# Optimization experiments

Measured on AMD Instinct MI355X. Metric: run time of the kernel, lower is better.

The kernel has to match this reference:

```python
import jax, jax.numpy as jnp
import numpy as np

PARAM = 10.0
EPS = 1e-10

def delu(x):
    # delu_feature_map: param*relu(x) + (exp(param*min(x,0)) - 1) + 1
    return PARAM * jax.nn.relu(x) + jnp.expm1(PARAM * jnp.minimum(x, 0.0)) + 1.0

def conv1x1(x, w, b):
    # x: (B,C,H,W), w: (O,C), b: (O,)
    return jnp.einsum('oc,bchw->bohw', w, x) + b[None, :, None, None]

def conv3x3(x, w, b):
    # x: (B,C,H,W), w: (O,C,3,3)
    y = jax.lax.conv_general_dilated(x, w, window_strides=(1, 1), padding='SAME',
                                     dimension_numbers=('NCHW', 'OIHW', 'NCHW'))
    return y + b[None, :, None, None]

def setup_inputs() -> dict:
    key = jax.random.key(0)
    B, C, H, W = 4, 256, 128, 128
    ks = jax.random.split(key, 20)
    s = 0.05
    d = {
        'x1': jax.random.normal(ks[0], (B, C, H, W), jnp.float32),
        'x2': jax.random.normal(ks[1], (B, C, H, W), jnp.float32),
        'wq1': jax.random.normal(ks[2], (C, C), jnp.float32) * s,
        'bq1': jax.random.normal(ks[3], (C,), jnp.float32) * s,
        'wk1': jax.random.normal(ks[4], (C, C), jnp.float32) * s,
        'bk1': jax.random.normal(ks[5], (C,), jnp.float32) * s,
        'wv1': jax.random.normal(ks[6], (C, C), jnp.float32) * s,
        'bv1': jax.random.normal(ks[7], (C,), jnp.float32) * s,
        'wq2': jax.random.normal(ks[8], (C, C), jnp.float32) * s,
        'bq2': jax.random.normal(ks[9], (C,), jnp.float32) * s,
        'wk2': jax.random.normal(ks[10], (C, C), jnp.float32) * s,
        'bk2': jax.random.normal(ks[11], (C,), jnp.float32) * s,
        'wv2': jax.random.normal(ks[12], (C, C), jnp.float32) * s,
        'bv2': jax.random.normal(ks[13], (C,), jnp.float32) * s,
        'wd1': jax.random.normal(ks[14], (C, C), jnp.float32) * s,
        'bd1': jax.random.normal(ks[15], (C,), jnp.float32) * s,
        'wd3': jax.random.normal(ks[16], (C, C, 3, 3), jnp.float32) * s,
        'bd3': jax.random.normal(ks[17], (C,), jnp.float32) * s,
        'gamma1': jax.random.normal(ks[18], (1,), jnp.float32) * 0.5,
        'gamma2': jax.random.normal(ks[19], (1,), jnp.float32) * 0.5,
    }
    return d

def reference(x1, x2, wq1, bq1, wk1, bk1, wv1, bv1, wq2, bq2, wk2, bk2,
              wv2, bv2, wd1, bd1, wd3, bd3, gamma1, gamma2):
    B, C, H, W = x1.shape
    N = H * W
    # QKV projections (1x1 convs), flattened to (B,C,N). delu is elementwise,
    # so applying it on (B,C,N) equals the permute/delu/permute in torch.
    q1 = delu(conv1x1(x1, wq1, bq1).reshape(B, C, N))
    k1 = delu(conv1x1(x1, wk1, bk1).reshape(B, C, N))
    v1 = conv1x1(x1, wv1, bv1).reshape(B, C, N)
    q2 = delu(conv1x1(x2, wq2, bq2).reshape(B, C, N))
    k2 = delu(conv1x1(x2, wk2, bk2).reshape(B, C, N))
    v2 = conv1x1(x2, wv2, bv2).reshape(B, C, N)

    # energy: (B,C,C) cross-kernel matrices
    energy1 = jnp.einsum('bmn,bcn->bmc', q1, k2)
    energy2 = jnp.einsum('bmn,bcn->bmc', q2, k1)

    KV1 = k1 * v1  # (B,C,N)
    KV2 = k2 * v2

    # norm: 1 / (sum_{m,c} energy[b,m,c] * k[b,c,n] + eps) -> (B,N)
    esum1 = energy1.sum(axis=1)  # (B,C)
    esum2 = energy2.sum(axis=1)
    norm1 = 1.0 / (jnp.einsum('bc,bcn->bn', esum1, k2) + EPS)
    norm2 = 1.0 / (jnp.einsum('bc,bcn->bn', esum2, k1) + EPS)

    # einsum('bmc,bcn,bn->bcn') factorizes: sum over m hits only energy
    att1 = (esum1[:, :, None] * KV1 * norm1[:, None, :]).reshape(B, C, H, W)
    att2 = (esum2[:, :, None] * KV2 * norm2[:, None, :]).reshape(B, C, H, W)

    out1 = att1 + conv1x1(x1, wd1, bd1) + conv3x3(x1, wd3, bd3)
    out2 = att2 + conv1x1(x2, wd1, bd1) + conv3x3(x2, wd3, bd3)
    out1 = x1 + gamma1[0] * out1
    out2 = x2 + gamma2[0] * out2
    return (out1, out2)
```

## Files before the change

### kernel.cpp

```cpp
#include <hip/hip_runtime.h>
#include <stdint.h>

#define Bn 4
#define Cn 256
#define Hn 128
#define Wn 128
#define Nn 16384
#define EPSn 1e-10f

typedef unsigned short u16;
typedef __attribute__((ext_vector_type(8))) short short8;
typedef __attribute__((ext_vector_type(4))) short short4v;
typedef __attribute__((ext_vector_type(4))) float f32x4;

#define GLOAD_LDS16(g, l)                                                        \
    __builtin_amdgcn_global_load_lds(                                            \
        (const __attribute__((address_space(1))) unsigned int*)(const void*)(g), \
        (__attribute__((address_space(3))) unsigned int*)(void*)(l), 16, 0, 0)

#define MFMA16(a, b, c) __builtin_amdgcn_mfma_f32_16x16x32_bf16(a, b, c, 0, 0, 0)

__device__ __forceinline__ float bf2f(u16 u) {
    union { float f; uint32_t i; } v; v.i = ((uint32_t)u) << 16; return v.f;
}
__device__ __forceinline__ u16 f2bf(float f) {
    union { float f; uint32_t i; } v; v.f = f;
    uint32_t r = v.i + 0x7FFFu + ((v.i >> 16) & 1u);
    return (u16)(r >> 16);
}
__device__ __forceinline__ float delu_f(float x) {
    return x >= 0.f ? fmaf(10.f, x, 1.f) : __expf(10.f * x);
}

__global__ void prep_kernel(const float* __restrict__ wq1, const float* __restrict__ wk1,
                            const float* __restrict__ wv1,
                            const float* __restrict__ wq2, const float* __restrict__ wk2,
                            const float* __restrict__ wv2,
                            const float* __restrict__ wd1, const float* __restrict__ wd3,
                            const float* __restrict__ bd1, const float* __restrict__ bd3,
                            const float* __restrict__ gamma1, const float* __restrict__ gamma2,
                            u16* __restrict__ wq1p, u16* __restrict__ wk1p, u16* __restrict__ wv1p,
                            u16* __restrict__ wq2p, u16* __restrict__ wk2p, u16* __restrict__ wv2p,
                            u16* __restrict__ wallp1, u16* __restrict__ wallp2,
                            float* __restrict__ bfused)
{
    int idx = blockIdx.x * 256 + threadIdx.x;
    int o = idx >> 8, c = idx & 255;
    if (idx < 256) bfused[idx] = bd1[idx] + bd3[idx];
    int s = o >> 6, mf = (o >> 4) & 3, lr = o & 15;
    int kc = c >> 5, lk = (c >> 3) & 3, j = c & 7;
    int poff = ((kc * 4 + s) * 4 + mf) * 512 + (lk * 16 + lr) * 8 + j;
    wq1p[poff] = f2bf(wq1[idx]);
    wk1p[poff] = f2bf(wk1[idx]);
    wv1p[poff] = f2bf(wv1[idx]);
    wq2p[poff] = f2bf(wq2[idx]);
    wk2p[poff] = f2bf(wk2[idx]);
    wv2p[poff] = f2bf(wv2[idx]);
    float wd1v = wd1[idx];
    float inv1 = 1.f / gamma1[0];
    float inv2 = 1.f / gamma2[0];
    float diag = (o == c) ? 1.f : 0.f;
    #pragma unroll
    for (int tap = 0; tap < 9; ++tap) {
        float w = wd3[idx * 9 + tap] + (tap == 4 ? wd1v : 0.f);
        wallp1[tap * 65536 + poff] = f2bf(w + (tap == 4 ? diag * inv1 : 0.f));
        wallp2[tap * 65536 + poff] = f2bf(w + (tap == 4 ? diag * inv2 : 0.f));
    }
}

__global__ void transpose_kernel(const float* __restrict__ x1, const float* __restrict__ x2,
                                 u16* __restrict__ xT1, u16* __restrict__ xT2)
{
    __shared__ __align__(16) u16 tl[64][72];
    int t = threadIdx.x;
    int z = blockIdx.z, img = z >> 2, b = z & 3;
    const float* x = img ? x2 : x1;
    u16* xT = img ? xT2 : xT1;
    int n0 = blockIdx.x * 64, c0 = blockIdx.y * 64;
    int cl = t >> 4, nl = (t & 15) * 4;
    #pragma unroll
    for (int pc = 0; pc < 4; ++pc) {
        int c = pc * 16 + cl;
        float4 v = *(const float4*)&x[((size_t)(b * Cn + c0 + c)) * Nn + n0 + nl];
        tl[nl + 0][c] = f2bf(v.x);
        tl[nl + 1][c] = f2bf(v.y);
        tl[nl + 2][c] = f2bf(v.z);
        tl[nl + 3][c] = f2bf(v.w);
    }
    __syncthreads();
    #pragma unroll
    for (int ps = 0; ps < 2; ++ps) {
        int id = ps * 256 + t;
        int nr = id >> 3, cc = (id & 7) * 8;
        short8 v = *(const short8*)&tl[nr][cc];
        *(short8*)&xT[((size_t)(b * Nn + n0 + nr)) * 256 + c0 + cc] = v;
    }
}

__global__ __launch_bounds__(256, 3) void qkv_kernel(
    const u16* __restrict__ xT1, const u16* __restrict__ xT2,
    const u16* __restrict__ wq1p, const u16* __restrict__ wk1p, const u16* __restrict__ wv1p,
    const u16* __restrict__ wq2p, const u16* __restrict__ wk2p, const u16* __restrict__ wv2p,
    const float* __restrict__ bq1, const float* __restrict__ bk1, const float* __restrict__ bv1,
    const float* __restrict__ bq2, const float* __restrict__ bk2, const float* __restrict__ bv2,
    u16* __restrict__ k1, u16* __restrict__ k2,
    u16* __restrict__ kv1, u16* __restrict__ kv2,
    float* __restrict__ qsum1, float* __restrict__ qsum2)
{
    __shared__ __align__(16) u16 Bt[2 * 2048];
    __shared__ __align__(16) u16 obuf[128 * 64];
    int t = threadIdx.x;
    int nb = blockIdx.x, mb = blockIdx.y;
    int z = blockIdx.z, img = z >> 2, b = z & 3;
    const u16* xT  = img ? xT2  : xT1;
    const u16* wqp = img ? wq2p : wq1p;
    const u16* wkp = img ? wk2p : wk1p;
    const u16* wvp = img ? wv2p : wv1p;
    const float* bq = img ? bq2 : bq1;
    const float* bk = img ? bk2 : bk1;
    const float* bv = img ? bv2 : bv1;
    u16* kout  = img ? k2  : k1;
    u16* kvout = img ? kv2 : kv1;
    float* qsum = img ? qsum2 : qsum1;

    int n0 = nb * 64;
    int lane = t & 63, wid = t >> 6;
    int wm = wid >> 1, wn = wid & 1;
    int lr = lane & 15, lk = lane >> 4;
    int s = mb * 2 + wm;

    f32x4 zf = {0.f, 0.f, 0.f, 0.f};
    f32x4 accq[4][2], acck[4][2], accv[4][2];
    #pragma unroll
    for (int i = 0; i < 4; ++i)
        #pragma unroll
        for (int j = 0; j < 2; ++j) { accq[i][j] = zf; acck[i][j] = zf; accv[i][j] = zf; }

    int colp = lane >> 2, chp = (lane & 3) * 8;
    auto STAGE = [&](int bufi, int kc) {
        const u16* g = xT + ((size_t)(b * Nn + n0 + wid * 16 + colp)) * 256 + kc * 32 + chp;
        GLOAD_LDS16(g, &Bt[bufi * 2048 + (wid * 16) * 32]);
    };

    STAGE(0, 0);
    __syncthreads();

    for (int kc = 0; kc < 8; ++kc) {
        int cur = kc & 1;
        if (kc < 7) STAGE(cur ^ 1, kc + 1);
        int abase = ((kc * 4 + s) * 4) * 512 + lane * 8;
        short8 bf[2];
        #pragma unroll
        for (int nf = 0; nf < 2; ++nf)
            bf[nf] = *(const short8*)&Bt[cur * 2048 + (wn * 32 + nf * 16 + lr) * 32 + lk * 8];
        #pragma unroll
        for (int mf = 0; mf < 4; ++mf) {
            short8 aq = *(const short8*)&wqp[abase + mf * 512];
            short8 ak = *(const short8*)&wkp[abase + mf * 512];
            short8 av = *(const short8*)&wvp[abase + mf * 512];
            __builtin_amdgcn_s_setprio(1);
            #pragma unroll
            for (int nf = 0; nf < 2; ++nf) {
                accq[mf][nf] = MFMA16(aq, bf[nf], accq[mf][nf]);
                acck[mf][nf] = MFMA16(ak, bf[nf], acck[mf][nf]);
                accv[mf][nf] = MFMA16(av, bf[nf], accv[mf][nf]);
            }
            __builtin_amdgcn_s_setprio(0);
        }
        __syncthreads();
    }

    float qs[2] = {0.f, 0.f};
    #pragma unroll
    for (int mf = 0; mf < 4; ++mf) {
        #pragma unroll
        for (int r = 0; r < 4; ++r) {
            int o = mb * 128 + wm * 64 + mf * 16 + lk * 4 + r;
            float bqv = bq[o];
            #pragma unroll
            for (int nf = 0; nf < 2; ++nf)
                qs[nf] += delu_f(accq[mf][nf][r] + bqv);
        }
    }
    #pragma unroll
    for (int nf = 0; nf < 2; ++nf) {
        float sgl = qs[nf];
        sgl += __shfl_xor(sgl, 16);
        sgl += __shfl_xor(sgl, 32);
        if (lk == 0)
            atomicAdd(&qsum[b * Nn + n0 + wn * 32 + nf * 16 + lr], sgl);
    }

    #pragma unroll
    for (int mf = 0; mf < 4; ++mf) {
        #pragma unroll
        for (int r = 0; r < 4; ++r) {
            int ol = wm * 64 + mf * 16 + lk * 4 + r;
            float bkv = bk[mb * 128 + ol];
            #pragma unroll
            for (int nf = 0; nf < 2; ++nf)
                obuf[ol * 64 + wn * 32 + nf * 16 + lr] = f2bf(delu_f(acck[mf][nf][r] + bkv));
        }
    }
    __syncthreads();
    #pragma unroll
    for (int i = 0; i < 4; ++i) {
        int sid = t * 4 + i;
        int o = sid >> 3, seg = sid & 7;
        short8 v = *(const short8*)&obuf[o * 64 + seg * 8];
        *(short8*)&kout[((size_t)(b * Cn + mb * 128 + o)) * Nn + n0 + seg * 8] = v;
    }
    __syncthreads();

    #pragma unroll
    for (int mf = 0; mf < 4; ++mf) {
        #pragma unroll
        for (int r = 0; r < 4; ++r) {
            int ol = wm * 64 + mf * 16 + lk * 4 + r;
            float bkv = bk[mb * 128 + ol];
            float bvv = bv[mb * 128 + ol];
            #pragma unroll
            for (int nf = 0; nf < 2; ++nf) {
                float kk = delu_f(acck[mf][nf][r] + bkv);
                float vv = accv[mf][nf][r] + bvv;
                obuf[ol * 64 + wn * 32 + nf * 16 + lr] = f2bf(kk * vv);
            }
        }
    }
    __syncthreads();
    #pragma unroll
    for (int i = 0; i < 4; ++i) {
        int sid = t * 4 + i;
        int o = sid >> 3, seg = sid & 7;
        short8 v = *(const short8*)&obuf[o * 64 + seg * 8];
        *(short8*)&kvout[((size_t)(b * Cn + mb * 128 + o)) * Nn + n0 + seg * 8] = v;
    }
}

__global__ void esum_kernel(const u16* __restrict__ k1, const u16* __restrict__ k2,
                            const float* __restrict__ qsum1, const float* __restrict__ qsum2,
                            float* __restrict__ esum1, float* __restrict__ esum2)
{
    int c = blockIdx.x, b = blockIdx.y, pair = blockIdx.z, t = threadIdx.x;
    const u16* k = pair ? k1 : k2;
    const float* qsum = pair ? qsum2 : qsum1;
    float* esum = pair ? esum2 : esum1;
    const u16* kr = k + ((size_t)(b * Cn + c)) * Nn;
    const float* qr = qsum + b * Nn;
    float s = 0.f;
    for (int i = t * 8; i < Nn; i += 2048) {
        short8 kv = *(const short8*)&kr[i];
        #pragma unroll
        for (int j = 0; j < 8; ++j) s = fmaf(bf2f((u16)kv[j]), qr[i + j], s);
    }
    #pragma unroll
    for (int m = 32; m; m >>= 1) s += __shfl_xor(s, m);
    __shared__ float red[4];
    if ((t & 63) == 0) red[t >> 6] = s;
    __syncthreads();
    if (t == 0) esum[b * Cn + c] = red[0] + red[1] + red[2] + red[3];
}

__global__ void norm_kernel(const u16* __restrict__ k1, const u16* __restrict__ k2,
                            const float* __restrict__ esum1, const float* __restrict__ esum2,
                            float* __restrict__ norm1, float* __restrict__ norm2)
{
    __shared__ float es[256];
    int t = threadIdx.x, b = blockIdx.y, pair = blockIdx.z;
    const u16* k = pair ? k1 : k2;
    const float* esum = pair ? esum2 : esum1;
    float* nrm = pair ? norm2 : norm1;
    es[t] = esum[b * Cn + t];
    __syncthreads();
    int n = blockIdx.x * 256 + t;
    const u16* kb = k + (size_t)b * Cn * Nn + n;
    float a = 0.f;
    #pragma unroll 8
    for (int c = 0; c < 256; ++c)
        a = fmaf(es[c], bf2f(kb[(size_t)c * Nn]), a);
    nrm[b * Nn + n] = 1.f / (a + EPSn);
}

#define BSZ6 (6 * 130 * 32)

__global__ __launch_bounds__(512, 2) void conv_att_kernel(
    const u16* __restrict__ xT,
    const u16* __restrict__ wallp, const float* __restrict__ bfused,
    const u16* __restrict__ kv, const float* __restrict__ esum,
    const float* __restrict__ nrm, const float* __restrict__ gamma,
    float* __restrict__ out)
{
    __shared__ __align__(16) u16 Bl[2 * BSZ6];
    int t = threadIdx.x;
    int lin = (blockIdx.z * 32 + blockIdx.y) * 2 + blockIdx.x;
    int xcd = lin & 7, slot = lin >> 3;
    int b = xcd >> 1;
    int ys = (xcd & 1) * 16 + (slot >> 1);
    int mb = slot & 1;
    int ybase = ys * 4;
    int lane = t & 63, wid = t >> 6;
    int wm = wid & 1, wy = wid >> 1;
    int lr = lane & 15, lk = lane >> 4;
    int s = mb * 2 + wm;

    f32x4 zf = {0.f, 0.f, 0.f, 0.f};
    f32x4 acc[4][8];
    #pragma unroll
    for (int i = 0; i < 4; ++i)
        #pragma unroll
        for (int j = 0; j < 8; ++j) acc[i][j] = zf;

    if (t < 96) {
        int buf = t / 48, r = t % 48;
        int row = r >> 3, pos = ((r >> 2) & 1) ? 129 : 0, q = r & 3;
        short8 z = {0, 0, 0, 0, 0, 0, 0, 0};
        *(short8*)&Bl[buf * BSZ6 + (row * 130 + pos) * 32 + q * 8] = z;
    }

    int colp = lane >> 2, chp = (lane & 3) * 8;
    auto STAGE = [&](int bufi, int kc) {
        #pragma unroll
        for (int i = 0; i < 6; ++i) {
            int run = wid * 6 + i;
            int hy = run >> 3, sx = run & 7;
            int yy = ybase + hy - 1;
            int dst = bufi * BSZ6 + (hy * 130 + 1 + sx * 16) * 32;
            if (yy < 0 || yy >= Hn) {
                short8 z = {0, 0, 0, 0, 0, 0, 0, 0};
                *(short8*)&Bl[dst + lane * 8] = z;
            } else {
                const u16* g = xT + ((size_t)(b * Nn + yy * Wn + sx * 16 + colp)) * 256
                                  + kc * 32 + chp;
                GLOAD_LDS16(g, &Bl[dst]);
            }
        }
    };

    STAGE(0, 0);
    __syncthreads();

    for (int kc = 0; kc < 8; ++kc) {
        int cur = kc & 1;
        int abase = ((kc * 4 + s) * 4) * 512 + lane * 8;
        short8 af[3][4];
        #pragma unroll
        for (int mf = 0; mf < 4; ++mf)
            af[0][mf] = *(const short8*)&wallp[0 * 65536 + abase + mf * 512];
        #pragma unroll
        for (int mf = 0; mf < 4; ++mf)
            af[1][mf] = *(const short8*)&wallp[1 * 65536 + abase + mf * 512];
        if (kc < 7) STAGE(cur ^ 1, kc + 1);
        int cb = cur * BSZ6;
        #pragma unroll
        for (int tap = 0; tap < 9; ++tap) {
            if (tap < 7) {
                #pragma unroll
                for (int mf = 0; mf < 4; ++mf)
                    af[(tap + 2) % 3][mf] =
                        *(const short8*)&wallp[(tap + 2) * 65536 + abase + mf * 512];
            }
            int dy = tap / 3, dx = tap % 3;
            short8 bf[8];
            #pragma unroll
            for (int nf = 0; nf < 8; ++nf)
                bf[nf] = *(const short8*)&Bl[cb + ((wy + dy) * 130 + nf * 16 + lr + dx) * 32 + lk * 8];
            __builtin_amdgcn_s_setprio(1);
            #pragma unroll
            for (int mf = 0; mf < 4; ++mf) {
                #pragma unroll
                for (int nf = 0; nf < 8; ++nf)
                    acc[mf][nf] = MFMA16(af[tap % 3][mf], bf[nf], acc[mf][nf]);
            }
            __builtin_amdgcn_s_setprio(0);
        }
        __syncthreads();
    }

    float g = gamma[0];
    int y = ybase + wy;
    int nbase = y * Wn;
    float nr8[8];
    #pragma unroll
    for (int nf = 0; nf < 8; ++nf)
        nr8[nf] = nrm[b * Nn + nbase + nf * 16 + lr];
    #pragma unroll
    for (int mf = 0; mf < 4; ++mf) {
        #pragma unroll
        for (int r = 0; r < 4; ++r) {
            int o = mb * 128 + wm * 64 + mf * 16 + lk * 4 + r;
            float es_o = esum[b * Cn + o];
            float bf_o = bfused[o];
            size_t rowbase = ((size_t)(b * Cn + o)) * Nn + nbase;
            #pragma unroll
            for (int nf = 0; nf < 8; ++nf) {
                size_t idx = rowbase + nf * 16 + lr;
                float att = es_o * bf2f(kv[idx]) * nr8[nf];
                out[idx] = g * (acc[mf][nf][r] + bf_o + att);
            }
        }
    }
}

extern "C" void kernel_launch(void* const* d_in, const int* in_sizes, int n_in,
                              void* d_out, int out_size, void* d_ws, size_t ws_size,
                              hipStream_t stream)
{
    const float* x1  = (const float*)d_in[0];
    const float* x2  = (const float*)d_in[1];
    const float* wq1 = (const float*)d_in[2];
    const float* bq1 = (const float*)d_in[3];
    const float* wk1 = (const float*)d_in[4];
    const float* bk1 = (const float*)d_in[5];
    const float* wv1 = (const float*)d_in[6];
    const float* bv1 = (const float*)d_in[7];
    const float* wq2 = (const float*)d_in[8];
    const float* bq2 = (const float*)d_in[9];
    const float* wk2 = (const float*)d_in[10];
    const float* bk2 = (const float*)d_in[11];
    const float* wv2 = (const float*)d_in[12];
    const float* bv2 = (const float*)d_in[13];
    const float* wd1 = (const float*)d_in[14];
    const float* bd1 = (const float*)d_in[15];
    const float* wd3 = (const float*)d_in[16];
    const float* bd3 = (const float*)d_in[17];
    const float* gamma1 = (const float*)d_in[18];
    const float* gamma2 = (const float*)d_in[19];

    char* ws = (char*)d_ws;
    size_t off = 0;
    auto alloc = [&](size_t bytes) { char* p = ws + off; off += (bytes + 255) & ~(size_t)255; return p; };

    u16* xT1    = (u16*)alloc((size_t)Bn * Nn * Cn * 2);
    u16* xT2    = (u16*)alloc((size_t)Bn * Nn * Cn * 2);
    u16* k1     = (u16*)alloc((size_t)Bn * Cn * Nn * 2);
    u16* k2     = (u16*)alloc((size_t)Bn * Cn * Nn * 2);
    u16* kv2    = (u16*)alloc((size_t)Bn * Cn * Nn * 2);
    u16* wallp1 = (u16*)alloc((size_t)9 * 65536 * 2);
    u16* wallp2 = (u16*)alloc((size_t)9 * 65536 * 2);
    u16* wq1p   = (u16*)alloc(65536 * 2);
    u16* wk1p   = (u16*)alloc(65536 * 2);
    u16* wv1p   = (u16*)alloc(65536 * 2);
    u16* wq2p   = (u16*)alloc(65536 * 2);
    u16* wk2p   = (u16*)alloc(65536 * 2);
    u16* wv2p   = (u16*)alloc(65536 * 2);
    float* qsum1 = (float*)alloc(Bn * Nn * 4);
    float* qsum2 = (float*)alloc(Bn * Nn * 4);
    float* esum1 = (float*)alloc(Bn * Cn * 4);
    float* esum2 = (float*)alloc(Bn * Cn * 4);
    float* norm1 = (float*)alloc(Bn * Nn * 4);
    float* norm2 = (float*)alloc(Bn * Nn * 4);
    float* bfused = (float*)alloc(Cn * 4);

    float* out1 = (float*)d_out;
    float* out2 = out1 + (size_t)Bn * Cn * Nn;
    u16* kv1 = (u16*)out2;

    hipMemsetAsync(qsum1, 0, Bn * Nn * 4, stream);
    hipMemsetAsync(qsum2, 0, Bn * Nn * 4, stream);

    prep_kernel<<<dim3(256), dim3(256), 0, stream>>>(wq1, wk1, wv1, wq2, wk2, wv2, wd1, wd3,
                                                     bd1, bd3, gamma1, gamma2,
                                                     wq1p, wk1p, wv1p, wq2p, wk2p, wv2p,
                                                     wallp1, wallp2, bfused);
    transpose_kernel<<<dim3(256, 4, 8), 256, 0, stream>>>(x1, x2, xT1, xT2);
    qkv_kernel<<<dim3(256, 2, 8), 256, 0, stream>>>(xT1, xT2,
                                                    wq1p, wk1p, wv1p, wq2p, wk2p, wv2p,
                                                    bq1, bk1, bv1, bq2, bk2, bv2,
                                                    k1, k2, kv1, kv2, qsum1, qsum2);
    esum_kernel<<<dim3(256, 4, 2), 256, 0, stream>>>(k1, k2, qsum1, qsum2, esum1, esum2);
    norm_kernel<<<dim3(64, 4, 2), 256, 0, stream>>>(k1, k2, esum1, esum2, norm1, norm2);
    conv_att_kernel<<<dim3(2, 32, 4), 512, 0, stream>>>(xT1, wallp1, bfused, kv1,
                                                        esum1, norm1, gamma1, out1);
    conv_att_kernel<<<dim3(2, 32, 4), 512, 0, stream>>>(xT2, wallp2, bfused, kv2,
                                                        esum2, norm2, gamma2, out2);
}
```

Before: 354.2 us.

## Preload full K tile into LDS and merge K/KV epilogue into one padded pass

The qkv kernel now issues all eight async global-to-LDS loads of the activation tile up front, replacing the double-buffered loop that synchronized every K-chunk. The main loop then runs fully unrolled with a single barrier at the end. The epilogue writes both delu(k) and k*v into one padded LDS buffer (row stride 68) in a single pass and uses coalesced sid mapping for the stores, dropping two barriers and a duplicate delu computation. LDS use rises to about 34 KB per block, which may reduce occupancy under launch_bounds(256,3).

```diff
diff --git a/kernel.cpp b/kernel.cpp
--- a/kernel.cpp
+++ b/kernel.cpp
@@ -97,6 +97,8 @@
     }
 }
 
+#define QK_LDS (2 * 128 * 68)
+
 __global__ __launch_bounds__(256, 3) void qkv_kernel(
     const u16* __restrict__ xT1, const u16* __restrict__ xT2,
     const u16* __restrict__ wq1p, const u16* __restrict__ wk1p, const u16* __restrict__ wv1p,
@@ -107,8 +109,7 @@
     u16* __restrict__ kv1, u16* __restrict__ kv2,
     float* __restrict__ qsum1, float* __restrict__ qsum2)
 {
-    __shared__ __align__(16) u16 Bt[2 * 2048];
-    __shared__ __align__(16) u16 obuf[128 * 64];
+    __shared__ __align__(16) u16 lds[QK_LDS];
     int t = threadIdx.x;
     int nb = blockIdx.x, mb = blockIdx.y;
     int z = blockIdx.z, img = z >> 2, b = z & 3;
@@ -137,38 +138,34 @@
         for (int j = 0; j < 2; ++j) { accq[i][j] = zf; acck[i][j] = zf; accv[i][j] = zf; }
 
     int colp = lane >> 2, chp = (lane & 3) * 8;
-    auto STAGE = [&](int bufi, int kc) {
+    #pragma unroll
+    for (int kc = 0; kc < 8; ++kc) {
         const u16* g = xT + ((size_t)(b * Nn + n0 + wid * 16 + colp)) * 256 + kc * 32 + chp;
-        GLOAD_LDS16(g, &Bt[bufi * 2048 + (wid * 16) * 32]);
-    };
-
-    STAGE(0, 0);
-    __syncthreads();
-
+        GLOAD_LDS16(g, &lds[kc * 2048 + (wid * 16) * 32]);
+    }
+    __syncthreads();
+
+    #pragma unroll
     for (int kc = 0; kc < 8; ++kc) {
-        int cur = kc & 1;
-        if (kc < 7) STAGE(cur ^ 1, kc + 1);
         int abase = ((kc * 4 + s) * 4) * 512 + lane * 8;
-        short8 bf[2];
-        #pragma unroll
-        for (int nf = 0; nf < 2; ++nf)
-            bf[nf] = *(const short8*)&Bt[cur * 2048 + (wn * 32 + nf * 16 + lr) * 32 + lk * 8];
+        short8 bf0 = *(const short8*)&lds[kc * 2048 + (wn * 32 + 0 * 16 + lr) * 32 + lk * 8];
+        short8 bf1 = *(const short8*)&lds[kc * 2048 + (wn * 32 + 1 * 16 + lr) * 32 + lk * 8];
         #pragma unroll
         for (int mf = 0; mf < 4; ++mf) {
             short8 aq = *(const short8*)&wqp[abase + mf * 512];
             short8 ak = *(const short8*)&wkp[abase + mf * 512];
             short8 av = *(const short8*)&wvp[abase + mf * 512];
             __builtin_amdgcn_s_setprio(1);
-            #pragma unroll
-            for (int nf = 0; nf < 2; ++nf) {
-                accq[mf][nf] = MFMA16(aq, bf[nf], accq[mf][nf]);
-                acck[mf][nf] = MFMA16(ak, bf[nf], acck[mf][nf]);
-                accv[mf][nf] = MFMA16(av, bf[nf], accv[mf][nf]);
-            }
+            accq[mf][0] = MFMA16(aq, bf0, accq[mf][0]);
+            accq[mf][1] = MFMA16(aq, bf1, accq[mf][1]);
+            acck[mf][0] = MFMA16(ak, bf0, acck[mf][0]);
+            acck[mf][1] = MFMA16(ak, bf1, acck[mf][1]);
+            accv[mf][0] = MFMA16(av, bf0, accv[mf][0]);
+            accv[mf][1] = MFMA16(av, bf1, accv[mf][1]);
             __builtin_amdgcn_s_setprio(0);
         }
-        __syncthreads();
-    }
+    }
+    __syncthreads();
 
     float qs[2] = {0.f, 0.f};
     #pragma unroll
@@ -190,27 +187,6 @@
         if (lk == 0)
             atomicAdd(&qsum[b * Nn + n0 + wn * 32 + nf * 16 + lr], sgl);
     }
-
-    #pragma unroll
-    for (int mf = 0; mf < 4; ++mf) {
-        #pragma unroll
-        for (int r = 0; r < 4; ++r) {
-            int ol = wm * 64 + mf * 16 + lk * 4 + r;
-            float bkv = bk[mb * 128 + ol];
-            #pragma unroll
-            for (int nf = 0; nf < 2; ++nf)
-                obuf[ol * 64 + wn * 32 + nf * 16 + lr] = f2bf(delu_f(acck[mf][nf][r] + bkv));
-        }
-    }
-    __syncthreads();
-    #pragma unroll
-    for (int i = 0; i < 4; ++i) {
-        int sid = t * 4 + i;
-        int o = sid >> 3, seg = sid & 7;
-        short8 v = *(const short8*)&obuf[o * 64 + seg * 8];
-        *(short8*)&kout[((size_t)(b * Cn + mb * 128 + o)) * Nn + n0 + seg * 8] = v;
-    }
-    __syncthreads();
 
     #pragma unroll
     for (int mf = 0; mf < 4; ++mf) {
@@ -223,16 +199,26 @@
             for (int nf = 0; nf < 2; ++nf) {
                 float kk = delu_f(acck[mf][nf][r] + bkv);
                 float vv = accv[mf][nf][r] + bvv;
-                obuf[ol * 64 + wn * 32 + nf * 16 + lr] = f2bf(kk * vv);
+                int col = wn * 32 + nf * 16 + lr;
+                lds[ol * 68 + col] = f2bf(kk);
+                lds[128 * 68 + ol * 68 + col] = f2bf(kk * vv);
             }
         }
     }
     __syncthreads();
+
     #pragma unroll
     for (int i = 0; i < 4; ++i) {
-        int sid = t * 4 + i;
+        int sid = i * 256 + t;
         int o = sid >> 3, seg = sid & 7;
-        short8 v = *(const short8*)&obuf[o * 64 + seg * 8];
+        short8 v = *(const short8*)&lds[o * 68 + seg * 8];
+        *(short8*)&kout[((size_t)(b * Cn + mb * 128 + o)) * Nn + n0 + seg * 8] = v;
+    }
+    #pragma unroll
+    for (int i = 0; i < 4; ++i) {
+        int sid = i * 256 + t;
+        int o = sid >> 3, seg = sid & 7;
+        short8 v = *(const short8*)&lds[128 * 68 + o * 68 + seg * 8];
         *(short8*)&kvout[((size_t)(b * Cn + mb * 128 + o)) * Nn + n0 + seg * 8] = v;
     }
 }
```

Result: faster. 332.1 us (-6.2%).
